# Optimization experiments

Hardware: AMD Instinct MI355X
Metric: run time of the kernel (lower is better)

Reference implementation:

```python
import jax, jax.numpy as jnp
import numpy as np

WS = 8
NH = 6

def _ln(x, g, b, eps=1e-5):
    m = jnp.mean(x, axis=-1, keepdims=True)
    v = jnp.var(x, axis=-1, keepdims=True)
    return (x - m) * jax.lax.rsqrt(v + eps) * g + b

def setup_inputs() -> dict:
    key = jax.random.key(0)
    ks = jax.random.split(key, 6)
    B, H, W, C = 4, 256, 256, 192
    s = 0.02
    return {
        "x": jax.random.normal(ks[0], (B, H, W, C), jnp.float32),
        "g1": jnp.ones((C,), jnp.float32),
        "b1": jnp.zeros((C,), jnp.float32),
        "w_qkv": jax.random.normal(ks[1], (C, 3 * C), jnp.float32) * s,
        "b_qkv": jnp.zeros((3 * C,), jnp.float32),
        "w_proj": jax.random.normal(ks[2], (C, C), jnp.float32) * s,
        "b_proj": jnp.zeros((C,), jnp.float32),
        "g2": jnp.ones((C,), jnp.float32),
        "b2": jnp.zeros((C,), jnp.float32),
        "w_fc1": jax.random.normal(ks[3], (C, 4 * C), jnp.float32) * s,
        "b_fc1": jnp.zeros((4 * C,), jnp.float32),
        "w_fc2": jax.random.normal(ks[4], (4 * C, C), jnp.float32) * s,
        "b_fc2": jnp.zeros((C,), jnp.float32),
    }

def reference(x, g1, b1, w_qkv, b_qkv, w_proj, b_proj, g2, b2, w_fc1, b_fc1, w_fc2, b_fc2):
    B, H, W, C = x.shape
    ws, nh = WS, NH
    hd = C // nh
    scale = hd ** -0.5
    N = ws * ws
    # window partition: (B,H,W,C) -> (B*nW, N, C). H,W divisible by ws, so pad branch is a no-op.
    xw = x.reshape(B, H // ws, ws, W // ws, ws, C).transpose(0, 1, 3, 2, 4, 5).reshape(-1, N, C)
    h = _ln(xw, g1, b1)
    qkv = h @ w_qkv + b_qkv                      # (Bn, N, 3C)
    q, k, v = jnp.split(qkv, 3, axis=-1)
    q = q.reshape(-1, N, nh, hd)
    k = k.reshape(-1, N, nh, hd)
    v = v.reshape(-1, N, nh, hd)
    attn = jax.nn.softmax(jnp.einsum('bnhd,bmhd->bhnm', q, k) * scale, axis=-1)
    o = jnp.einsum('bhnm,bmhd->bnhd', attn, v).reshape(-1, N, C)
    xw = xw + (o @ w_proj + b_proj)              # residual inside windows
    # window unpartition: (B*nW, N, C) -> (B, H, W, C)
    xo = xw.reshape(B, H // ws, W // ws, ws, ws, C).transpose(0, 1, 3, 2, 4, 5).reshape(B, H, W, C)
    h2 = _ln(xo, g2, b2)
    h2 = jax.nn.gelu(h2 @ w_fc1 + b_fc1, approximate=False) @ w_fc2 + b_fc2
    return xo + h2
```

## Files before the change

kernel.cpp:

```cpp
#include <hip/hip_runtime.h>
#include <hip/hip_bf16.h>

typedef unsigned short u16;
typedef __attribute__((ext_vector_type(8))) short short8;
typedef __attribute__((ext_vector_type(4))) short short4v;
typedef __attribute__((ext_vector_type(4))) float f32x4;
typedef __attribute__((ext_vector_type(16))) float f32x16;

__device__ __forceinline__ u16 f2bf(float f){
  __hip_bfloat16 h = __float2bfloat16(f);
  return *reinterpret_cast<u16*>(&h);
}

__device__ __forceinline__ float gelu_fast(float u){
  float uu = u * u;
  float e = __expf(u * fmaf(uu, -0.0713548163f, -1.5957691216f));
  return u * __builtin_amdgcn_rcpf(1.f + e);
}

__global__ void transpose_all(const float* __restrict__ w0, u16* __restrict__ d0,
                              const float* __restrict__ w1, u16* __restrict__ d1,
                              const float* __restrict__ w2, u16* __restrict__ d2,
                              const float* __restrict__ w3, u16* __restrict__ d3)
{
  int seg = blockIdx.y;
  int idx = blockIdx.x * 256 + threadIdx.x;
  if (seg == 0){
    if (idx < 192 * 576){ int k = idx / 576, n = idx % 576; d0[n * 192 + k] = f2bf(w0[idx]); }
  } else if (seg == 1){
    if (idx < 192 * 192){ int k = idx / 192, n = idx % 192; d1[n * 192 + k] = f2bf(w1[idx]); }
  } else if (seg == 2){
    if (idx < 192 * 768){
      int k = idx / 768, n = idx % 768;
      d2[(size_t)(n >> 6) * 12800 + (n & 63) * 200 + k] = f2bf(w2[idx]);
    }
  } else {
    if (idx < 768 * 192){
      int k = idx / 192, n = idx % 192;
      d3[(size_t)(k >> 6) * 13824 + n * 72 + (k & 63)] = f2bf(w3[idx]);
    }
  }
}

__global__ __launch_bounds__(256, 2) void win_attn(
    const float* __restrict__ x,  const float* __restrict__ g1, const float* __restrict__ b1,
    const u16* __restrict__ wqkvT, const float* __restrict__ bqkv,
    const u16* __restrict__ wprojT, const float* __restrict__ bproj,
    float* __restrict__ out)
{
  __shared__ u16 hw[64 * 200];
  __shared__ u16 wch[96 * 200];
  u16* Ql = wch;
  u16* Kl = wch + 64 * 40;
  u16* Vt = Kl  + 64 * 40;
  u16* Pl = Vt  + 32 * 72;

  const int tid = threadIdx.x, lane = tid & 63, w = tid >> 6;
  const int l15 = lane & 15, quad = lane >> 4;
  const int wid = blockIdx.x;
  const int b = wid >> 10, hy = (wid >> 5) & 31, wx = wid & 31;

  {
    int n = w * 16 + (lane >> 2), p = lane & 3;
    int hr = hy * 8 + (n >> 3), wcc = wx * 8 + (n & 7);
    size_t tg = ((size_t)(b * 256 + hr)) * 256 + wcc;
    const float* xr = x + tg * 192 + p * 48;
    float v[48];
    #pragma unroll
    for (int c = 0; c < 12; c++) *(float4*)(v + c * 4) = *(const float4*)(xr + c * 4);
    float s = 0.f, ss = 0.f;
    #pragma unroll
    for (int i = 0; i < 48; i++){ s += v[i]; ss += v[i] * v[i]; }
    s += __shfl_xor(s, 1); ss += __shfl_xor(ss, 1);
    s += __shfl_xor(s, 2); ss += __shfl_xor(ss, 2);
    float m  = s * (1.f / 192.f);
    float rs = rsqrtf(ss * (1.f / 192.f) - m * m + 1e-5f);
    #pragma unroll
    for (int c = 0; c < 12; c++){
      float4 gv = *(const float4*)(g1 + p * 48 + c * 4);
      float4 bv = *(const float4*)(b1 + p * 48 + c * 4);
      short4v t;
      t.x = (short)f2bf((v[c*4+0] - m) * rs * gv.x + bv.x);
      t.y = (short)f2bf((v[c*4+1] - m) * rs * gv.y + bv.y);
      t.z = (short)f2bf((v[c*4+2] - m) * rs * gv.z + bv.z);
      t.w = (short)f2bf((v[c*4+3] - m) * rs * gv.w + bv.w);
      *(short4v*)&hw[n * 200 + p * 48 + c * 4] = t;
    }
  }

  const int qrow = w * 16 + quad * 4;
  f32x4 oall[6][2];
  #pragma unroll
  for (int h = 0; h < 6; h++)
    #pragma unroll
    for (int nt = 0; nt < 2; nt++) oall[h][nt] = (f32x4){0.f, 0.f, 0.f, 0.f};

  #pragma unroll
  for (int head = 0; head < 6; ++head){
    __syncthreads();
    #pragma unroll
    for (int it = 0; it < 9; ++it){
      int c = tid + it * 256;
      int row = c / 24, cc = c % 24;
      int gr = (row >> 5) * 192 + head * 32 + (row & 31);
      *(uint4*)&wch[row * 200 + cc * 8] = *(const uint4*)(wqkvT + (size_t)gr * 192 + cc * 8);
    }
    __syncthreads();
    f32x4 acc[3][2];
    #pragma unroll
    for (int mat = 0; mat < 3; mat++)
      #pragma unroll
      for (int nt = 0; nt < 2; nt++) acc[mat][nt] = (f32x4){0.f, 0.f, 0.f, 0.f};
    #pragma unroll
    for (int k = 0; k < 6; k++){
      short8 af = *(const short8*)&hw[(w * 16 + l15) * 200 + k * 32 + quad * 8];
      #pragma unroll
      for (int mat = 0; mat < 3; mat++)
        #pragma unroll
        for (int nt = 0; nt < 2; nt++){
          short8 bfv = *(const short8*)&wch[(mat * 32 + nt * 16 + l15) * 200 + k * 32 + quad * 8];
          acc[mat][nt] = __builtin_amdgcn_mfma_f32_16x16x32_bf16(af, bfv, acc[mat][nt], 0, 0, 0);
        }
    }
    __syncthreads();
    #pragma unroll
    for (int nt = 0; nt < 2; nt++){
      float bq = bqkv[      head * 32 + nt * 16 + l15];
      float bk = bqkv[192 + head * 32 + nt * 16 + l15];
      float bv = bqkv[384 + head * 32 + nt * 16 + l15];
      #pragma unroll
      for (int r = 0; r < 4; r++){
        Ql[(qrow + r) * 40 + nt * 16 + l15] = f2bf(acc[0][nt][r] + bq);
        Kl[(qrow + r) * 40 + nt * 16 + l15] = f2bf(acc[1][nt][r] + bk);
        Vt[(nt * 16 + l15) * 72 + qrow + r] = f2bf(acc[2][nt][r] + bv);
      }
    }
    __syncthreads();
    short8 aq = *(const short8*)&Ql[(w * 16 + l15) * 40 + quad * 8];
    f32x4 sa[4];
    #pragma unroll
    for (int kt = 0; kt < 4; kt++){
      short8 bk8 = *(const short8*)&Kl[(kt * 16 + l15) * 40 + quad * 8];
      sa[kt] = __builtin_amdgcn_mfma_f32_16x16x32_bf16(aq, bk8, (f32x4){0.f,0.f,0.f,0.f}, 0, 0, 0);
    }
    const float scale = 0.17677669529663687f;
    float inv[4];
    #pragma unroll
    for (int r = 0; r < 4; r++){
      float s0 = sa[0][r] * scale, s1 = sa[1][r] * scale;
      float s2 = sa[2][r] * scale, s3 = sa[3][r] * scale;
      float mx = fmaxf(fmaxf(s0, s1), fmaxf(s2, s3));
      mx = fmaxf(mx, __shfl_xor(mx, 1)); mx = fmaxf(mx, __shfl_xor(mx, 2));
      mx = fmaxf(mx, __shfl_xor(mx, 4)); mx = fmaxf(mx, __shfl_xor(mx, 8));
      float p0 = __expf(s0 - mx), p1 = __expf(s1 - mx);
      float p2 = __expf(s2 - mx), p3 = __expf(s3 - mx);
      float l = p0 + p1 + p2 + p3;
      l += __shfl_xor(l, 1); l += __shfl_xor(l, 2);
      l += __shfl_xor(l, 4); l += __shfl_xor(l, 8);
      inv[r] = 1.f / l;
      Pl[(qrow + r) * 72 +      l15] = f2bf(p0);
      Pl[(qrow + r) * 72 + 16 + l15] = f2bf(p1);
      Pl[(qrow + r) * 72 + 32 + l15] = f2bf(p2);
      Pl[(qrow + r) * 72 + 48 + l15] = f2bf(p3);
    }
    f32x4 oa[2];
    oa[0] = (f32x4){0.f,0.f,0.f,0.f}; oa[1] = (f32x4){0.f,0.f,0.f,0.f};
    #pragma unroll
    for (int ks = 0; ks < 2; ks++){
      short8 ap = *(const short8*)&Pl[(w * 16 + l15) * 72 + ks * 32 + quad * 8];
      #pragma unroll
      for (int nt = 0; nt < 2; nt++){
        short8 bv8 = *(const short8*)&Vt[(nt * 16 + l15) * 72 + ks * 32 + quad * 8];
        oa[nt] = __builtin_amdgcn_mfma_f32_16x16x32_bf16(ap, bv8, oa[nt], 0, 0, 0);
      }
    }
    #pragma unroll
    for (int nt = 0; nt < 2; nt++)
      #pragma unroll
      for (int r = 0; r < 4; r++)
        oall[head][nt][r] = oa[nt][r] * inv[r];
  }

  #pragma unroll
  for (int h = 0; h < 6; h++)
    #pragma unroll
    for (int nt = 0; nt < 2; nt++)
      #pragma unroll
      for (int r = 0; r < 4; r++)
        hw[(qrow + r) * 200 + h * 32 + nt * 16 + l15] = f2bf(oall[h][nt][r]);

  f32x4 accP[12];
  #pragma unroll
  for (int nt = 0; nt < 12; nt++) accP[nt] = (f32x4){0.f,0.f,0.f,0.f};
  #pragma unroll
  for (int k = 0; k < 6; k++){
    short8 af = *(const short8*)&hw[(w * 16 + l15) * 200 + k * 32 + quad * 8];
    #pragma unroll
    for (int nt = 0; nt < 12; nt++){
      short8 bfv = *(const short8*)(wprojT + (size_t)(nt * 16 + l15) * 192 + k * 32 + quad * 8);
      accP[nt] = __builtin_amdgcn_mfma_f32_16x16x32_bf16(af, bfv, accP[nt], 0, 0, 0);
    }
  }
  #pragma unroll
  for (int r = 0; r < 4; r++){
    int nn = qrow + r;
    int hr = hy * 8 + (nn >> 3), wcc = wx * 8 + (nn & 7);
    size_t tg = ((size_t)(b * 256 + hr)) * 256 + wcc;
    #pragma unroll
    for (int nt = 0; nt < 12; nt++){
      int col = nt * 16 + l15;
      size_t idx = tg * 192 + col;
      out[idx] = accP[nt][r] + bproj[col] + x[idx];
    }
  }
}

__global__ __launch_bounds__(256, 2) void mlp_fused(
    const float* __restrict__ g2, const float* __restrict__ b2,
    const u16* __restrict__ wfc1P, const float* __restrict__ bfc1,
    const u16* __restrict__ wfc2P, const float* __restrict__ bfc2,
    float* __restrict__ io)
{
  __shared__ u16 w1s[2][64 * 200];
  __shared__ u16 w2s[192 * 72];
  u16* h2t = w2s;

  const int tid = threadIdx.x, lane = tid & 63, w = tid >> 6;
  const int l15 = lane & 15, quad = lane >> 4;
  const int l31 = lane & 31, half = lane >> 5;
  const int wm = w >> 1, wn = w & 1;
  const int t0 = blockIdx.x * 64;

  typedef const __attribute__((address_space(1))) void gv_t;
  typedef __attribute__((address_space(3))) void lv_t;

  #define ISSUE_W1(ch, buf)                                                        \
    { const u16* src = wfc1P + (size_t)(ch) * 12800;                               \
      _Pragma("unroll")                                                            \
      for (int t = 0; t < 7; ++t){ int j = w + t * 4;                              \
        if (j < 25)                                                                \
          __builtin_amdgcn_global_load_lds((gv_t*)(src + j * 512 + lane * 8),      \
                                           (lv_t*)&w1s[buf][j * 512], 16, 0, 0); } }
  #define ISSUE_W2(ch)                                                             \
    { const u16* src = wfc2P + (size_t)(ch) * 13824;                               \
      _Pragma("unroll")                                                            \
      for (int t = 0; t < 7; ++t){ int j = w + t * 4;                              \
        if (j < 27)                                                                \
          __builtin_amdgcn_global_load_lds((gv_t*)(src + j * 512 + lane * 8),      \
                                           (lv_t*)&w2s[j * 512], 16, 0, 0); } }

  {
    int n = w * 16 + (lane >> 2), p = lane & 3;
    const float* xr = io + (size_t)(t0 + n) * 192 + p * 48;
    float v[48];
    #pragma unroll
    for (int c = 0; c < 12; c++) *(float4*)(v + c * 4) = *(const float4*)(xr + c * 4);
    float s = 0.f, ss = 0.f;
    #pragma unroll
    for (int i = 0; i < 48; i++){ s += v[i]; ss += v[i] * v[i]; }
    s += __shfl_xor(s, 1); ss += __shfl_xor(ss, 1);
    s += __shfl_xor(s, 2); ss += __shfl_xor(ss, 2);
    float m  = s * (1.f / 192.f);
    float rs = rsqrtf(ss * (1.f / 192.f) - m * m + 1e-5f);
    #pragma unroll
    for (int c = 0; c < 12; c++){
      float4 gv = *(const float4*)(g2 + p * 48 + c * 4);
      float4 bv = *(const float4*)(b2 + p * 48 + c * 4);
      short4v t;
      t.x = (short)f2bf((v[c*4+0] - m) * rs * gv.x + bv.x);
      t.y = (short)f2bf((v[c*4+1] - m) * rs * gv.y + bv.y);
      t.z = (short)f2bf((v[c*4+2] - m) * rs * gv.z + bv.z);
      t.w = (short)f2bf((v[c*4+3] - m) * rs * gv.w + bv.w);
      *(short4v*)&h2t[n * 200 + p * 48 + c * 4] = t;
    }
  }
  asm volatile("s_waitcnt lgkmcnt(0)\ns_barrier" ::: "memory");

  short8 afr[6];
  #pragma unroll
  for (int k = 0; k < 6; ++k)
    afr[k] = *(const short8*)&h2t[(w * 16 + l15) * 200 + k * 32 + quad * 8];
  asm volatile("s_waitcnt lgkmcnt(0)\ns_barrier" ::: "memory");

  ISSUE_W1(0, 0);
  ISSUE_W2(0);
  ISSUE_W1(1, 1);

  f32x16 accO[3];
  #pragma unroll
  for (int t = 0; t < 3; ++t)
    #pragma unroll
    for (int i = 0; i < 16; ++i) accO[t][i] = 0.f;

  #pragma unroll
  for (int ch = 0; ch < 12; ++ch){
    const int cur = ch & 1;
    if (ch < 11) asm volatile("s_waitcnt vmcnt(12) lgkmcnt(0)\ns_barrier" ::: "memory");
    else         asm volatile("s_waitcnt vmcnt(6) lgkmcnt(0)\ns_barrier" ::: "memory");

    f32x4 au[4];
    #pragma unroll
    for (int nt = 0; nt < 4; ++nt) au[nt] = (f32x4){0.f,0.f,0.f,0.f};
    #pragma unroll
    for (int k = 0; k < 6; ++k)
      #pragma unroll
      for (int nt = 0; nt < 4; ++nt){
        short8 bf = *(const short8*)&w1s[cur][(nt * 16 + l15) * 200 + k * 32 + quad * 8];
        au[nt] = __builtin_amdgcn_mfma_f32_16x16x32_bf16(afr[k], bf, au[nt], 0, 0, 0);
      }
    asm volatile("s_waitcnt lgkmcnt(0)\ns_barrier" ::: "memory");

    u16* Ut = &w1s[cur][0];
    #pragma unroll
    for (int nt = 0; nt < 4; ++nt){
      float bb = bfc1[ch * 64 + nt * 16 + l15];
      #pragma unroll
      for (int r = 0; r < 4; ++r)
        Ut[(w * 16 + quad * 4 + r) * 72 + nt * 16 + l15] = f2bf(gelu_fast(au[nt][r] + bb));
    }
    if (ch < 11) asm volatile("s_waitcnt vmcnt(6) lgkmcnt(0)\ns_barrier" ::: "memory");
    else         asm volatile("s_waitcnt vmcnt(0) lgkmcnt(0)\ns_barrier" ::: "memory");

    #pragma unroll
    for (int ks = 0; ks < 4; ++ks){
      short8 uf = *(const short8*)&Ut[(wm * 32 + l31) * 72 + ks * 16 + half * 8];
      #pragma unroll
      for (int t = 0; t < 3; ++t){
        short8 bf = *(const short8*)&w2s[(wn * 96 + t * 32 + l31) * 72 + ks * 16 + half * 8];
        accO[t] = __builtin_amdgcn_mfma_f32_32x32x16_bf16(uf, bf, accO[t], 0, 0, 0);
      }
    }
    asm volatile("s_waitcnt lgkmcnt(0)\ns_barrier" ::: "memory");

    if (ch < 11) ISSUE_W2(ch + 1);
    if (ch < 10) ISSUE_W1(ch + 2, cur);
  }

  #pragma unroll
  for (int t = 0; t < 3; ++t){
    int col = wn * 96 + t * 32 + l31;
    float bbo = bfc2[col];
    #pragma unroll
    for (int r = 0; r < 16; ++r){
      int row = t0 + wm * 32 + (r & 3) + 8 * (r >> 2) + 4 * half;
      size_t idx = (size_t)row * 192 + col;
      io[idx] = accO[t][r] + bbo + io[idx];
    }
  }
  #undef ISSUE_W1
  #undef ISSUE_W2
}

extern "C" void kernel_launch(void* const* d_in, const int* in_sizes, int n_in,
                              void* d_out, int out_size, void* d_ws, size_t ws_size,
                              hipStream_t stream) {
  const float* x      = (const float*)d_in[0];
  const float* g1     = (const float*)d_in[1];
  const float* b1     = (const float*)d_in[2];
  const float* w_qkv  = (const float*)d_in[3];
  const float* b_qkv  = (const float*)d_in[4];
  const float* w_proj = (const float*)d_in[5];
  const float* b_proj = (const float*)d_in[6];
  const float* g2     = (const float*)d_in[7];
  const float* b2     = (const float*)d_in[8];
  const float* w_fc1  = (const float*)d_in[9];
  const float* b_fc1  = (const float*)d_in[10];
  const float* w_fc2  = (const float*)d_in[11];
  const float* b_fc2  = (const float*)d_in[12];
  float* out = (float*)d_out;

  u16* wqkvT  = (u16*)d_ws;
  u16* wprojT = wqkvT  + 576 * 192;
  u16* wfc1P  = wprojT + 192 * 192;
  u16* wfc2P  = wfc1P  + 12 * 12800;

  transpose_all<<<dim3(576, 4), 256, 0, stream>>>(w_qkv, wqkvT, w_proj, wprojT,
                                                  w_fc1, wfc1P, w_fc2, wfc2P);
  win_attn<<<4096, 256, 0, stream>>>(x, g1, b1, wqkvT, b_qkv, wprojT, b_proj, out);
  mlp_fused<<<4096, 256, 0, stream>>>(g2, b2, wfc1P, b_fc1, wfc2P, b_fc2, out);
}
```

Measured before the change: 905.4 us.

## Prefetch per-head QKV weights into LDS asynchronously with global_load_lds

The QKV weights are now pre-packed per head into a padded layout that matches the LDS tile. While the current head's attention runs, the kernel issues asynchronous global-to-LDS loads for the next head's weight slice, instead of doing synchronous register-staged copies between barriers. The LayerNorm A-fragments are loaded into registers once and reused across all heads. The Q/K/V/P scratch tiles move into the hw buffer so the weight buffer can be refilled while attention runs. The risks are the hand-written waitcnt/barrier ordering, slightly more LDS use, and higher register pressure from the cached fragments.

```diff
diff --git a/kernel.cpp b/kernel.cpp
--- a/kernel.cpp
+++ b/kernel.cpp
@@ -26,7 +26,12 @@
   int seg = blockIdx.y;
   int idx = blockIdx.x * 256 + threadIdx.x;
   if (seg == 0){
-    if (idx < 192 * 576){ int k = idx / 576, n = idx % 576; d0[n * 192 + k] = f2bf(w0[idx]); }
+    if (idx < 192 * 576){
+      int k = idx / 576, n = idx % 576;
+      int mat = n / 192, r = n % 192;
+      int head = r >> 5, r32 = r & 31;
+      d0[(size_t)head * 19456 + (mat * 32 + r32) * 200 + k] = f2bf(w0[idx]);
+    }
   } else if (seg == 1){
     if (idx < 192 * 192){ int k = idx / 192, n = idx % 192; d1[n * 192 + k] = f2bf(w1[idx]); }
   } else if (seg == 2){
@@ -44,21 +49,34 @@
 
 __global__ __launch_bounds__(256, 2) void win_attn(
     const float* __restrict__ x,  const float* __restrict__ g1, const float* __restrict__ b1,
-    const u16* __restrict__ wqkvT, const float* __restrict__ bqkv,
+    const u16* __restrict__ wqkvP, const float* __restrict__ bqkv,
     const u16* __restrict__ wprojT, const float* __restrict__ bproj,
     float* __restrict__ out)
 {
   __shared__ u16 hw[64 * 200];
-  __shared__ u16 wch[96 * 200];
-  u16* Ql = wch;
-  u16* Kl = wch + 64 * 40;
-  u16* Vt = Kl  + 64 * 40;
-  u16* Pl = Vt  + 32 * 72;
+  __shared__ u16 wch[19456];
+  u16* Ql = hw;
+  u16* Kl = hw + 2560;
+  u16* Vt = hw + 5120;
+  u16* Pl = hw + 7424;
 
   const int tid = threadIdx.x, lane = tid & 63, w = tid >> 6;
   const int l15 = lane & 15, quad = lane >> 4;
   const int wid = blockIdx.x;
   const int b = wid >> 10, hy = (wid >> 5) & 31, wx = wid & 31;
+
+  typedef const __attribute__((address_space(1))) void gv_t;
+  typedef __attribute__((address_space(3))) void lv_t;
+
+  #define ISSUE_QKV(h)                                                           \
+    { const u16* src = wqkvP + (size_t)(h) * 19456;                              \
+      _Pragma("unroll")                                                          \
+      for (int t = 0; t < 10; ++t){ int j = w + t * 4;                           \
+        if (j < 38)                                                              \
+          __builtin_amdgcn_global_load_lds((gv_t*)(src + j * 512 + lane * 8),    \
+                                           (lv_t*)&wch[j * 512], 16, 0, 0); } }
+
+  ISSUE_QKV(0);
 
   {
     int n = w * 16 + (lane >> 2), p = lane & 3;
@@ -87,6 +105,12 @@
       *(short4v*)&hw[n * 200 + p * 48 + c * 4] = t;
     }
   }
+  asm volatile("s_waitcnt lgkmcnt(0)\ns_barrier" ::: "memory");
+
+  short8 afr[6];
+  #pragma unroll
+  for (int k = 0; k < 6; ++k)
+    afr[k] = *(const short8*)&hw[(w * 16 + l15) * 200 + k * 32 + quad * 8];
 
   const int qrow = w * 16 + quad * 4;
   f32x4 oall[6][2];
@@ -97,32 +121,25 @@
 
   #pragma unroll
   for (int head = 0; head < 6; ++head){
-    __syncthreads();
-    #pragma unroll
-    for (int it = 0; it < 9; ++it){
-      int c = tid + it * 256;
-      int row = c / 24, cc = c % 24;
-      int gr = (row >> 5) * 192 + head * 32 + (row & 31);
-      *(uint4*)&wch[row * 200 + cc * 8] = *(const uint4*)(wqkvT + (size_t)gr * 192 + cc * 8);
-    }
-    __syncthreads();
+    asm volatile("s_waitcnt vmcnt(0) lgkmcnt(0)\ns_barrier" ::: "memory");
+
     f32x4 acc[3][2];
     #pragma unroll
     for (int mat = 0; mat < 3; mat++)
       #pragma unroll
       for (int nt = 0; nt < 2; nt++) acc[mat][nt] = (f32x4){0.f, 0.f, 0.f, 0.f};
     #pragma unroll
-    for (int k = 0; k < 6; k++){
-      short8 af = *(const short8*)&hw[(w * 16 + l15) * 200 + k * 32 + quad * 8];
+    for (int k = 0; k < 6; k++)
       #pragma unroll
       for (int mat = 0; mat < 3; mat++)
         #pragma unroll
         for (int nt = 0; nt < 2; nt++){
           short8 bfv = *(const short8*)&wch[(mat * 32 + nt * 16 + l15) * 200 + k * 32 + quad * 8];
-          acc[mat][nt] = __builtin_amdgcn_mfma_f32_16x16x32_bf16(af, bfv, acc[mat][nt], 0, 0, 0);
+          acc[mat][nt] = __builtin_amdgcn_mfma_f32_16x16x32_bf16(afr[k], bfv, acc[mat][nt], 0, 0, 0);
         }
-    }
-    __syncthreads();
+    asm volatile("s_waitcnt lgkmcnt(0)\ns_barrier" ::: "memory");
+
+    if (head < 5) ISSUE_QKV(head + 1);
     #pragma unroll
     for (int nt = 0; nt < 2; nt++){
       float bq = bqkv[      head * 32 + nt * 16 + l15];
@@ -135,7 +152,8 @@
         Vt[(nt * 16 + l15) * 72 + qrow + r] = f2bf(acc[2][nt][r] + bv);
       }
     }
-    __syncthreads();
+    asm volatile("s_waitcnt lgkmcnt(0)\ns_barrier" ::: "memory");
+
     short8 aq = *(const short8*)&Ql[(w * 16 + l15) * 40 + quad * 8];
     f32x4 sa[4];
     #pragma unroll
@@ -181,6 +199,8 @@
         oall[head][nt][r] = oa[nt][r] * inv[r];
   }
 
+  asm volatile("s_waitcnt lgkmcnt(0)\ns_barrier" ::: "memory");
+
   #pragma unroll
   for (int h = 0; h < 6; h++)
     #pragma unroll
@@ -213,6 +233,7 @@
       out[idx] = accP[nt][r] + bproj[col] + x[idx];
     }
   }
+  #undef ISSUE_QKV
 }
 
 __global__ __launch_bounds__(256, 2) void mlp_fused(
@@ -369,13 +390,13 @@
   const float* b_fc2  = (const float*)d_in[12];
   float* out = (float*)d_out;
 
-  u16* wqkvT  = (u16*)d_ws;
-  u16* wprojT = wqkvT  + 576 * 192;
+  u16* wqkvP  = (u16*)d_ws;
+  u16* wprojT = wqkvP  + 6 * 19456;
   u16* wfc1P  = wprojT + 192 * 192;
   u16* wfc2P  = wfc1P  + 12 * 12800;
 
-  transpose_all<<<dim3(576, 4), 256, 0, stream>>>(w_qkv, wqkvT, w_proj, wprojT,
+  transpose_all<<<dim3(576, 4), 256, 0, stream>>>(w_qkv, wqkvP, w_proj, wprojT,
                                                   w_fc1, wfc1P, w_fc2, wfc2P);
-  win_attn<<<4096, 256, 0, stream>>>(x, g1, b1, wqkvT, b_qkv, wprojT, b_proj, out);
+  win_attn<<<4096, 256, 0, stream>>>(x, g1, b1, wqkvP, b_qkv, wprojT, b_proj, out);
   mlp_fused<<<4096, 256, 0, stream>>>(g2, b2, wfc1P, b_fc1, wfc2P, b_fc2, out);
 }
```

Measured after the change: 888.4 us. About the same (-1.9%).
